# Performance work log

Measured on AMD Instinct MI355X. Metric: run time of the kernel, lower is better.

The kernel has to match this reference:

```python
import jax, jax.numpy as jnp
import numpy as np

B, T, D_IN, H, NUM_CLASSES = 1024, 512, 4, 64, 3
G = 4 * H  # gates: i, f, g, o (PyTorch order)


def setup_inputs() -> dict:
    key = jax.random.key(0)
    ks = jax.random.split(key, 32)
    s = 0.1  # small init scale, like PyTorch's 1/sqrt(H) uniform
    inp = {"x": jax.random.normal(ks[0], (B, T, D_IN), jnp.float32)}
    i = 1
    for l in range(4):
        d = D_IN if l == 0 else H
        inp[f"w_ih_{l}"] = s * jax.random.normal(ks[i], (G, d), jnp.float32); i += 1
        inp[f"w_hh_{l}"] = s * jax.random.normal(ks[i], (G, H), jnp.float32); i += 1
        inp[f"b_ih_{l}"] = s * jax.random.normal(ks[i], (G,), jnp.float32); i += 1
        inp[f"b_hh_{l}"] = s * jax.random.normal(ks[i], (G,), jnp.float32); i += 1
    inp["fc1_w"] = s * jax.random.normal(ks[i], (H // 2, H), jnp.float32); i += 1
    inp["fc1_b"] = s * jax.random.normal(ks[i], (H // 2,), jnp.float32); i += 1
    inp["fc2_w"] = s * jax.random.normal(ks[i], (NUM_CLASSES, H // 2), jnp.float32); i += 1
    inp["fc2_b"] = s * jax.random.normal(ks[i], (NUM_CLASSES,), jnp.float32)
    return inp


def _lstm_layer(x, w_ih, w_hh, b_ih, b_hh):
    # x: [B, T, d_in] -> [B, T, H]; PyTorch gate order i, f, g, o.
    b, t, _ = x.shape
    # Precompute input contribution for all timesteps in one GEMM.
    pre = jnp.einsum('btd,gd->tbg', x, w_ih) + (b_ih + b_hh)  # [T, B, 4H]
    h0 = jnp.zeros((b, H), x.dtype)
    c0 = jnp.zeros((b, H), x.dtype)

    def step(carry, p):
        h, c = carry
        gates = p + h @ w_hh.T  # [B, 4H]
        i_g, f_g, g_g, o_g = jnp.split(gates, 4, axis=-1)
        i_g = jax.nn.sigmoid(i_g)
        f_g = jax.nn.sigmoid(f_g)
        g_g = jnp.tanh(g_g)
        o_g = jax.nn.sigmoid(o_g)
        c = f_g * c + i_g * g_g
        h = o_g * jnp.tanh(c)
        return (h, c), h

    _, hs = jax.lax.scan(step, (h0, c0), pre)  # hs: [T, B, H]
    return hs.transpose(1, 0, 2)


def reference(x,
              w_ih_0, w_hh_0, b_ih_0, b_hh_0,
              w_ih_1, w_hh_1, b_ih_1, b_hh_1,
              w_ih_2, w_hh_2, b_ih_2, b_hh_2,
              w_ih_3, w_hh_3, b_ih_3, b_hh_3,
              fc1_w, fc1_b, fc2_w, fc2_b):
    layers = [(w_ih_0, w_hh_0, b_ih_0, b_hh_0),
              (w_ih_1, w_hh_1, b_ih_1, b_hh_1),
              (w_ih_2, w_hh_2, b_ih_2, b_hh_2),
              (w_ih_3, w_hh_3, b_ih_3, b_hh_3)]
    h = x
    for (wi, wh, bi, bh) in layers:
        h = _lstm_layer(h, wi, wh, bi, bh)
    last = h[:, -1, :]                         # [B, H]
    z = jax.nn.relu(last @ fc1_w.T + fc1_b)    # [B, H//2]
    logits = z @ fc2_w.T + fc2_b               # [B, 3]
    return jax.nn.softmax(logits, axis=1)
```

## Files before the change

### kernel.cpp

```cpp
#include <hip/hip_runtime.h>


#define TLEN 512
#define NCH  64
#define AG   __HIP_MEMORY_SCOPE_AGENT
#define SPIN_CAP 2000000
#define LOG2E 1.44269504f
#define TWOLOG2E 2.88539008f

typedef __bf16 bf16x8 __attribute__((ext_vector_type(8)));
typedef float  f32x4  __attribute__((ext_vector_type(4)));

struct Params {
  const float* x;
  const float* wih[4]; const float* whh[4];
  const float* bih[4]; const float* bhh[4];
  const float* fc1w; const float* fc1b;
  const float* fc2w; const float* fc2b;
  float* out; char* ws;
  int CAP; int CM;
};

__device__ __forceinline__ bf16x8 bfzero() {
  union { unsigned long long u[2]; bf16x8 v; } z; z.u[0] = 0ull; z.u[1] = 0ull; return z.v;
}
__device__ __forceinline__ float fast_sigmoid(float x) {
  return __builtin_amdgcn_rcpf(1.f + __expf(-x));
}
__device__ __forceinline__ float fast_tanh(float x) {
  float e = __expf(2.f * x);
  return 1.f - 2.f * __builtin_amdgcn_rcpf(e + 1.f);
}
__device__ __forceinline__ void load_frag_pair(const unsigned short* sb, int l15, int quad,
                                               bf16x8& f0, bf16x8& f1) {
  const unsigned long long* a = (const unsigned long long*)(sb + l15 * 64 + quad * 8);
  const unsigned long long* b = (const unsigned long long*)(sb + l15 * 64 + 32 + quad * 8);
  union { bf16x8 v; unsigned long long u[2]; } c0, c1;
  c0.u[0] = __hip_atomic_load(&a[0], __ATOMIC_RELAXED, AG);
  c0.u[1] = __hip_atomic_load(&a[1], __ATOMIC_RELAXED, AG);
  c1.u[0] = __hip_atomic_load(&b[0], __ATOMIC_RELAXED, AG);
  c1.u[1] = __hip_atomic_load(&b[1], __ATOMIC_RELAXED, AG);
  f0 = c0.v; f1 = c1.v;
}

__global__ __launch_bounds__(512, 1) void lstm_split(Params p)
{
  const int bid   = blockIdx.x;
  const int role  = bid >> 6;
  const int chunk = bid & 63;
  const int b0    = chunk * 16;
  const int tid   = threadIdx.x;
  const int wave  = tid >> 6;
  const int grp   = wave >> 2;
  const int w     = wave & 3;
  const int lane  = tid & 63;
  const int quad  = lane >> 4;
  const int l15   = lane & 15;
  const int L     = role * 2 + grp;

  __shared__ __bf16 tiles[2][2][1024];
  __shared__ float  s_fc1w[2048];
  __shared__ float  s_z[512];
  __shared__ float  s_fc1b[32];
  __shared__ float  s_fc2w[96];
  __shared__ float  s_fc2b[3];

  int* flagp = (int*)p.ws + chunk * 16;
  int* ackp  = (int*)(p.ws + 16 * 1024) + chunk * 16;
  unsigned short* ringc = (unsigned short*)(p.ws + 32 * 1024) + (size_t)chunk * p.CAP * 1024;
  const int CAP = p.CAP, CM = p.CM;

  bf16x8 wf[4][4];
  float  bias[4];
  {
    const float gsc[4] = { -LOG2E, -LOG2E, TWOLOG2E, -LOG2E };
    const float* wih = p.wih[L];
    const float* whh = p.whh[L];
    const float* bih = p.bih[L];
    const float* bhh = p.bhh[L];
#pragma unroll
    for (int g = 0; g < 4; g++) {
      const float sc = gsc[g];
      int n = g * 64 + w * 16 + l15;
      bias[g] = (bih[n] + bhh[n]) * sc;
      if (L == 0) {
        bf16x8 f = bfzero();
        if (quad == 0) {
#pragma unroll
          for (int j = 0; j < 4; j++) f[j] = (__bf16)(wih[n * 4 + j] * sc);
        }
        wf[g][0] = f; wf[g][1] = bfzero();
      } else {
#pragma unroll
        for (int q = 0; q < 2; q++) {
          const float* s = wih + n * 64 + q * 32 + quad * 8;
          bf16x8 f;
#pragma unroll
          for (int j = 0; j < 8; j++) f[j] = (__bf16)(s[j] * sc);
          wf[g][q] = f;
        }
      }
#pragma unroll
      for (int q = 0; q < 2; q++) {
        const float* s = whh + n * 64 + q * 32 + quad * 8;
        bf16x8 f;
#pragma unroll
        for (int j = 0; j < 8; j++) f[j] = (__bf16)(s[j] * sc);
        wf[g][2 + q] = f;
      }
    }
  }

  { int* ti = (int*)tiles; for (int i = tid; i < 2048; i += 512) ti[i] = 0; }
  float cst[4] = {0.f, 0.f, 0.f, 0.f};

  int W = -1000000000, f_pend = -1000000000;
  int ackW = -1000000000, a_pend = -1000000000;
  bf16x8 xA0 = bfzero(), xA1 = bfzero();
  bf16x8 xB0 = bfzero(), xB1 = bfzero();
  bf16x8 xC0 = bfzero(), xC1 = bfzero();
  float4 xraw = {0.f, 0.f, 0.f, 0.f};

  if (role == 0) {
    if (grp == 0 && quad == 0) {
      const float* xb = p.x + (size_t)(b0 + l15) * TLEN * 4;
      const float4 x0 = *(const float4*)(xb);
      const float4 x1 = *(const float4*)(xb + 4);
      xraw = *(const float4*)(xb + 8);
      bf16x8 f = bfzero();
      f[0] = (__bf16)x0.x; f[1] = (__bf16)x0.y; f[2] = (__bf16)x0.z; f[3] = (__bf16)x0.w;
      xA0 = f;
      bf16x8 g = bfzero();
      g[0] = (__bf16)x1.x; g[1] = (__bf16)x1.y; g[2] = (__bf16)x1.z; g[3] = (__bf16)x1.w;
      xB0 = g;
    }
  } else if (grp == 0) {
    int v = -1000000000, it = 0;
    do {
      if (lane == 0) v = __hip_atomic_load(flagp, __ATOMIC_ACQUIRE, AG);
      v = __shfl(v, 0);
      if (v >= 10) break;
      __builtin_amdgcn_s_sleep(1);
    } while (++it < SPIN_CAP);
    W = v;
    load_frag_pair(ringc,        l15, quad, xA0, xA1);
    load_frag_pair(ringc + 1024, l15, quad, xB0, xB1);
    load_frag_pair(ringc + 2048, l15, quad, xC0, xC1);
  }
  __syncthreads();

  const int SMAX = (role == 0) ? (TLEN + 2) : (TLEN + 1);
  for (int s = 0; s < SMAX; s++) {
    const int t  = s - grp;
    const int pr = s & 1, pw = pr ^ 1;
    unsigned hb[4];

    if ((unsigned)t < (unsigned)TLEN) {
      bf16x8 if0, if1;
      if (grp == 0) { if0 = xA0; if1 = xA1; }
      else {
        const __bf16* src = tiles[pr][0];
        int sg0 = quad ^ (l15 & 7);
        int sg1 = (4 + quad) ^ (l15 & 7);
        if0 = *(const bf16x8*)&src[l15 * 64 + sg0 * 8];
        if1 = *(const bf16x8*)&src[l15 * 64 + sg1 * 8];
      }
      bf16x8 hf0, hf1;
      {
        const __bf16* src = tiles[pr][grp];
        int sg0 = quad ^ (l15 & 7);
        int sg1 = (4 + quad) ^ (l15 & 7);
        hf0 = *(const bf16x8*)&src[l15 * 64 + sg0 * 8];
        hf1 = *(const bf16x8*)&src[l15 * 64 + sg1 * 8];
      }

      f32x4 acc[4];
#pragma unroll
      for (int g = 0; g < 4; g++) { f32x4 a = {bias[g], bias[g], bias[g], bias[g]}; acc[g] = a; }
      if (L == 0) {
#pragma unroll
        for (int g = 0; g < 4; g++)
          acc[g] = __builtin_amdgcn_mfma_f32_16x16x32_bf16(if0, wf[g][0], acc[g], 0, 0, 0);
      } else {
#pragma unroll
        for (int g = 0; g < 4; g++) {
          acc[g] = __builtin_amdgcn_mfma_f32_16x16x32_bf16(if0, wf[g][0], acc[g], 0, 0, 0);
          acc[g] = __builtin_amdgcn_mfma_f32_16x16x32_bf16(if1, wf[g][1], acc[g], 0, 0, 0);
        }
      }
#pragma unroll
      for (int g = 0; g < 4; g++) {
        acc[g] = __builtin_amdgcn_mfma_f32_16x16x32_bf16(hf0, wf[g][2], acc[g], 0, 0, 0);
        acc[g] = __builtin_amdgcn_mfma_f32_16x16x32_bf16(hf1, wf[g][3], acc[g], 0, 0, 0);
      }

      const int col = w * 16 + l15;
      __bf16* dst = tiles[pw][grp];
#pragma unroll
      for (int r = 0; r < 4; r++) {
        float ig = __builtin_amdgcn_rcpf(1.f + __builtin_amdgcn_exp2f(acc[0][r]));
        float fg = __builtin_amdgcn_rcpf(1.f + __builtin_amdgcn_exp2f(acc[1][r]));
        float gg = 1.f - 2.f * __builtin_amdgcn_rcpf(1.f + __builtin_amdgcn_exp2f(acc[2][r]));
        float og = __builtin_amdgcn_rcpf(1.f + __builtin_amdgcn_exp2f(acc[3][r]));
        float c  = fg * cst[r] + ig * gg;
        cst[r] = c;
        float th = 1.f - 2.f * __builtin_amdgcn_rcpf(1.f + __builtin_amdgcn_exp2f(TWOLOG2E * c));
        float h  = og * th;
        __bf16 hbf = (__bf16)h;
        union { __bf16 b; unsigned short s; } cv; cv.b = hbf;
        hb[r] = cv.s;
        int m  = quad * 4 + r;
        int sg = (col >> 3) ^ (m & 7);
        dst[m * 64 + sg * 8 + (col & 7)] = hbf;
      }
    }

    __syncthreads();

    if (role == 0) {
      if (grp == 0) {
        xA0 = xB0;
        if (quad == 0) {
          bf16x8 f = bfzero();
          f[0] = (__bf16)xraw.x; f[1] = (__bf16)xraw.y;
          f[2] = (__bf16)xraw.z; f[3] = (__bf16)xraw.w;
          xB0 = f;
          if (t + 3 < TLEN)
            xraw = *(const float4*)(p.x + ((size_t)(b0 + l15) * TLEN + (t + 3)) * 4);
        }
      }
      if (grp == 1 && (unsigned)t < (unsigned)TLEN) {
        int am = __shfl(a_pend, 0);
        if (am > ackW) ackW = am;
        if (lane == 0) a_pend = __hip_atomic_load(ackp, __ATOMIC_RELAXED, AG);
        if (t >= CAP && ackW < t - CAP + 1) {
          int v = ackW, it = 0;
          do {
            if (lane == 0) v = __hip_atomic_load(ackp, __ATOMIC_ACQUIRE, AG);
            v = __shfl(v, 0);
            if (v >= t - CAP + 1) break;
            __builtin_amdgcn_s_sleep(1);
          } while (++it < SPIN_CAP);
          ackW = v;
        }
        const int col = w * 16 + l15;
        unsigned* rdst = (unsigned*)(ringc + (size_t)(t & CM) * 1024);
#pragma unroll
        for (int r = 0; r < 4; r++) {
          unsigned v = hb[r];
          unsigned o = (unsigned)__shfl_xor((int)v, 1);
          if ((lane & 1) == 0) {
            int m = quad * 4 + r;
            __hip_atomic_store(&rdst[(m * 64 + col) >> 1], v | (o << 16), __ATOMIC_RELAXED, AG);
          }
        }
      }
      if (tid == 0 && s >= 2)
        __hip_atomic_store(flagp, s - 1, __ATOMIC_RELAXED, AG);
    } else {
      if (grp == 0) {
        int fm = __shfl(f_pend, 0);
        if (fm > W) W = fm;
        if (lane == 0) f_pend = __hip_atomic_load(flagp, __ATOMIC_RELAXED, AG);
        xA0 = xB0; xA1 = xB1; xB0 = xC0; xB1 = xC1;
        if (t + 3 < TLEN) {
          if (W < t + 4) {
            int v = W, it = 0;
            do {
              if (lane == 0) v = __hip_atomic_load(flagp, __ATOMIC_ACQUIRE, AG);
              v = __shfl(v, 0);
              if (v >= t + 4) break;
              __builtin_amdgcn_s_sleep(1);
            } while (++it < SPIN_CAP);
            W = v;
          }
          load_frag_pair(ringc + (size_t)((t + 3) & CM) * 1024, l15, quad, xC0, xC1);
        }
      }
      if (tid == 0)
        __hip_atomic_store(ackp, s + 2, __ATOMIC_RELAXED, AG);
    }
  }

  if (role == 1) {
    for (int i = tid; i < 2048; i += 512) s_fc1w[i] = p.fc1w[i];
    if (tid < 32) s_fc1b[tid] = p.fc1b[tid];
    if (tid < 96) s_fc2w[tid] = p.fc2w[tid];
    if (tid < 3)  s_fc2b[tid] = p.fc2b[tid];
    __syncthreads();
    {
      int m = tid >> 5, u = tid & 31;
      float sacc = s_fc1b[u];
      const float* wrow = &s_fc1w[u * 64];
      const __bf16* hfin = tiles[1][1];
#pragma unroll
      for (int k = 0; k < 64; k++) {
        int sg = (k >> 3) ^ (m & 7);
        sacc += (float)hfin[m * 64 + sg * 8 + (k & 7)] * wrow[k];
      }
      s_z[m * 32 + u] = fmaxf(sacc, 0.f);
    }
    __syncthreads();
    if (tid < 16) {
      int m = tid;
      float lg[3];
#pragma unroll
      for (int v = 0; v < 3; v++) {
        float sv = s_fc2b[v];
#pragma unroll
        for (int u = 0; u < 32; u++) sv += s_z[m * 32 + u] * s_fc2w[v * 32 + u];
        lg[v] = sv;
      }
      float mx = fmaxf(lg[0], fmaxf(lg[1], lg[2]));
      float e0 = __expf(lg[0] - mx), e1 = __expf(lg[1] - mx), e2 = __expf(lg[2] - mx);
      float inv = 1.f / (e0 + e1 + e2);
      float* o = p.out + (size_t)(b0 + m) * 3;
      o[0] = e0 * inv; o[1] = e1 * inv; o[2] = e2 * inv;
    }
  }
}

__global__ __launch_bounds__(1024) void lstm_fused(Params p)
{
  const int chunk = blockIdx.x;
  const int b0   = chunk * 16;
  const int tid  = threadIdx.x;
  const int wave = tid >> 6;
  const int L    = wave >> 2;
  const int w    = wave & 3;
  const int lane = tid & 63;
  const int quad = lane >> 4;
  const int l15  = lane & 15;

  __shared__ __bf16 tiles[2][5][16 * 64];
  __shared__ float  s_fc1w[2048];
  __shared__ float  s_z[512];
  __shared__ float  s_fc1b[32];
  __shared__ float  s_fc2w[96];
  __shared__ float  s_fc2b[3];

  bf16x8 wf[4][4];
  float  bias[4];
  {
    const float* wih = p.wih[L];
    const float* whh = p.whh[L];
    const float* bih = p.bih[L];
    const float* bhh = p.bhh[L];
#pragma unroll
    for (int g = 0; g < 4; g++) {
      int n = g * 64 + w * 16 + l15;
      bias[g] = bih[n] + bhh[n];
      if (L == 0) {
        bf16x8 f = bfzero();
        if (quad == 0) {
#pragma unroll
          for (int j = 0; j < 4; j++) f[j] = (__bf16)wih[n * 4 + j];
        }
        wf[g][0] = f; wf[g][1] = bfzero();
      } else {
#pragma unroll
        for (int q = 0; q < 2; q++) {
          const float* s = wih + n * 64 + q * 32 + quad * 8;
          bf16x8 f;
#pragma unroll
          for (int j = 0; j < 8; j++) f[j] = (__bf16)s[j];
          wf[g][q] = f;
        }
      }
#pragma unroll
      for (int q = 0; q < 2; q++) {
        const float* s = whh + n * 64 + q * 32 + quad * 8;
        bf16x8 f;
#pragma unroll
        for (int j = 0; j < 8; j++) f[j] = (__bf16)s[j];
        wf[g][2 + q] = f;
      }
    }
  }

  { int* ti = (int*)tiles; for (int i = tid; i < 5120; i += 1024) ti[i] = 0; }
  float cst[4] = {0.f, 0.f, 0.f, 0.f};

  if (wave == 0 && quad == 0) {
    const float4 xv = *(const float4*)(p.x + ((size_t)(b0 + l15) * TLEN) * 4);
    __bf16 v[4] = {(__bf16)xv.x, (__bf16)xv.y, (__bf16)xv.z, (__bf16)xv.w};
    *(float2*)&tiles[0][0][l15 * 64 + (l15 & 7) * 8] = *(float2*)v;
  }
  __syncthreads();

  for (int s = 0; s < TLEN + 3; s++) {
    const int t  = s - L;
    const int pr = s & 1;
    const int pw = pr ^ 1;

    if ((unsigned)t < (unsigned)TLEN) {
      const __bf16* in  = tiles[pr][L];
      const __bf16* own = tiles[pr][L + 1];
      const int sg0 = quad ^ (l15 & 7);
      const int sg1 = (4 + quad) ^ (l15 & 7);
      bf16x8 xf0 = *(const bf16x8*)&in [l15 * 64 + sg0 * 8];
      bf16x8 xf1 = *(const bf16x8*)&in [l15 * 64 + sg1 * 8];
      bf16x8 hf0 = *(const bf16x8*)&own[l15 * 64 + sg0 * 8];
      bf16x8 hf1 = *(const bf16x8*)&own[l15 * 64 + sg1 * 8];

      f32x4 acc[4];
#pragma unroll
      for (int g = 0; g < 4; g++) { f32x4 a = {bias[g], bias[g], bias[g], bias[g]}; acc[g] = a; }
#pragma unroll
      for (int g = 0; g < 4; g++) {
        acc[g] = __builtin_amdgcn_mfma_f32_16x16x32_bf16(xf0, wf[g][0], acc[g], 0, 0, 0);
        acc[g] = __builtin_amdgcn_mfma_f32_16x16x32_bf16(xf1, wf[g][1], acc[g], 0, 0, 0);
        acc[g] = __builtin_amdgcn_mfma_f32_16x16x32_bf16(hf0, wf[g][2], acc[g], 0, 0, 0);
        acc[g] = __builtin_amdgcn_mfma_f32_16x16x32_bf16(hf1, wf[g][3], acc[g], 0, 0, 0);
      }

      if (wave == 0 && quad == 0 && t + 1 < TLEN) {
        const float4 xv = *(const float4*)(p.x + ((size_t)(b0 + l15) * TLEN + (t + 1)) * 4);
        __bf16 v[4] = {(__bf16)xv.x, (__bf16)xv.y, (__bf16)xv.z, (__bf16)xv.w};
        *(float2*)&tiles[pw][0][l15 * 64 + (l15 & 7) * 8] = *(float2*)v;
      }

      const int col = w * 16 + l15;
      __bf16* dst = tiles[pw][L + 1];
#pragma unroll
      for (int r = 0; r < 4; r++) {
        float ig = fast_sigmoid(acc[0][r]);
        float fg = fast_sigmoid(acc[1][r]);
        float gg = fast_tanh(acc[2][r]);
        float og = fast_sigmoid(acc[3][r]);
        float c = fg * cst[r] + ig * gg;
        cst[r] = c;
        float h = og * fast_tanh(c);
        int m  = quad * 4 + r;
        int sg = (col >> 3) ^ (m & 7);
        dst[m * 64 + sg * 8 + (col & 7)] = (__bf16)h;
      }
    }
    __syncthreads();
  }

  for (int i = tid; i < 2048; i += 1024) s_fc1w[i] = p.fc1w[i];
  if (tid < 32) s_fc1b[tid] = p.fc1b[tid];
  if (tid < 96) s_fc2w[tid] = p.fc2w[tid];
  if (tid < 3)  s_fc2b[tid] = p.fc2b[tid];
  __syncthreads();
  if (tid < 512) {
    int m = tid >> 5, u = tid & 31;
    float sacc = s_fc1b[u];
    const float* wrow = &s_fc1w[u * 64];
    const __bf16* hfin = tiles[1][4];
#pragma unroll
    for (int k = 0; k < 64; k++) {
      int sg = (k >> 3) ^ (m & 7);
      sacc += (float)hfin[m * 64 + sg * 8 + (k & 7)] * wrow[k];
    }
    s_z[m * 32 + u] = fmaxf(sacc, 0.f);
  }
  __syncthreads();
  if (tid < 16) {
    int m = tid;
    float lg[3];
#pragma unroll
    for (int v = 0; v < 3; v++) {
      float sv = s_fc2b[v];
#pragma unroll
      for (int u = 0; u < 32; u++) sv += s_z[m * 32 + u] * s_fc2w[v * 32 + u];
      lg[v] = sv;
    }
    float mx = fmaxf(lg[0], fmaxf(lg[1], lg[2]));
    float e0 = __expf(lg[0] - mx), e1 = __expf(lg[1] - mx), e2 = __expf(lg[2] - mx);
    float inv = 1.f / (e0 + e1 + e2);
    float* o = p.out + (size_t)(b0 + m) * 3;
    o[0] = e0 * inv; o[1] = e1 * inv; o[2] = e2 * inv;
  }
}

extern "C" void kernel_launch(void* const* d_in, const int* in_sizes, int n_in,
                              void* d_out, int out_size, void* d_ws, size_t ws_size,
                              hipStream_t stream)
{
  (void)in_sizes; (void)n_in; (void)out_size;
  Params p;
  p.x = (const float*)d_in[0];
  for (int l = 0; l < 4; l++) {
    p.wih[l] = (const float*)d_in[1 + 4 * l];
    p.whh[l] = (const float*)d_in[2 + 4 * l];
    p.bih[l] = (const float*)d_in[3 + 4 * l];
    p.bhh[l] = (const float*)d_in[4 + 4 * l];
  }
  p.fc1w = (const float*)d_in[17];
  p.fc1b = (const float*)d_in[18];
  p.fc2w = (const float*)d_in[19];
  p.fc2b = (const float*)d_in[20];
  p.out = (float*)d_out;
  p.ws  = (char*)d_ws;

  const size_t avail = (ws_size > 32768) ? (ws_size - 32768) : 0;
  int CAP = 1;
  while (CAP < 64 && (size_t)(CAP * 2) * (NCH * 2048ull) <= avail) CAP <<= 1;

  if (CAP >= 16) {
    p.CAP = CAP; p.CM = CAP - 1;
    hipLaunchKernelGGL(lstm_split, dim3(128), dim3(512), 65536, stream, p);
  } else {
    p.CAP = 0; p.CM = 0;
    hipLaunchKernelGGL(lstm_fused, dim3(NCH), dim3(1024), 0, stream, p);
  }
}
```

Before: 881.0 us.

## Process two batch chunks per block in split LSTM kernel

The two-role pipelined LSTM kernel now handles two 16-row batch chunks per block, so the grid shrinks from 128 to 64 blocks. Each block interleaves two independent recurrences per timestep, which lets MFMA and transcendental latency of one chunk overlap with the other, and one flag/ack handshake now covers both chunks. The cost is a longer per-step critical path, more registers and shared memory per block, and fewer CUs in use. The forced 64 KB dynamic shared-memory allocation is dropped and the spin cap is lowered.

Result: slower. 1.314 ms (+49.2%).

```diff
diff --git a/kernel.cpp b/kernel.cpp
--- a/kernel.cpp
+++ b/kernel.cpp
@@ -4,7 +4,7 @@
 #define TLEN 512
 #define NCH  64
 #define AG   __HIP_MEMORY_SCOPE_AGENT
-#define SPIN_CAP 2000000
+#define SPIN_CAP 1500000
 #define LOG2E 1.44269504f
 #define TWOLOG2E 2.88539008f
 
@@ -43,12 +43,11 @@
   f0 = c0.v; f1 = c1.v;
 }
 
-__global__ __launch_bounds__(512, 1) void lstm_split(Params p)
+__global__ __launch_bounds__(512, 1) void lstm_split2(Params p)
 {
   const int bid   = blockIdx.x;
-  const int role  = bid >> 6;
-  const int chunk = bid & 63;
-  const int b0    = chunk * 16;
+  const int role  = bid >> 5;
+  const int k     = bid & 31;
   const int tid   = threadIdx.x;
   const int wave  = tid >> 6;
   const int grp   = wave >> 2;
@@ -57,17 +56,21 @@
   const int quad  = lane >> 4;
   const int l15   = lane & 15;
   const int L     = role * 2 + grp;
-
-  __shared__ __bf16 tiles[2][2][1024];
+  const int cc[2] = { k, k + 32 };
+
+  __shared__ __bf16 tiles[2][2][2][1024];
   __shared__ float  s_fc1w[2048];
-  __shared__ float  s_z[512];
+  __shared__ float  s_z[1024];
   __shared__ float  s_fc1b[32];
   __shared__ float  s_fc2w[96];
   __shared__ float  s_fc2b[3];
 
-  int* flagp = (int*)p.ws + chunk * 16;
-  int* ackp  = (int*)(p.ws + 16 * 1024) + chunk * 16;
-  unsigned short* ringc = (unsigned short*)(p.ws + 32 * 1024) + (size_t)chunk * p.CAP * 1024;
+  int* flagp = (int*)p.ws + cc[0] * 16;
+  int* ackp  = (int*)(p.ws + 16 * 1024) + cc[0] * 16;
+  unsigned short* ringb = (unsigned short*)(p.ws + 32 * 1024);
+  unsigned short* ring[2];
+  ring[0] = ringb + (size_t)cc[0] * p.CAP * 1024;
+  ring[1] = ringb + (size_t)cc[1] * p.CAP * 1024;
   const int CAP = p.CAP, CM = p.CM;
 
   bf16x8 wf[4][4];
@@ -111,28 +114,36 @@
     }
   }
 
-  { int* ti = (int*)tiles; for (int i = tid; i < 2048; i += 512) ti[i] = 0; }
-  float cst[4] = {0.f, 0.f, 0.f, 0.f};
+  { int* ti = (int*)tiles; for (int i = tid; i < 4096; i += 512) ti[i] = 0; }
+  float cst[2][4] = {{0.f,0.f,0.f,0.f},{0.f,0.f,0.f,0.f}};
 
   int W = -1000000000, f_pend = -1000000000;
   int ackW = -1000000000, a_pend = -1000000000;
-  bf16x8 xA0 = bfzero(), xA1 = bfzero();
-  bf16x8 xB0 = bfzero(), xB1 = bfzero();
-  bf16x8 xC0 = bfzero(), xC1 = bfzero();
-  float4 xraw = {0.f, 0.f, 0.f, 0.f};
+  bf16x8 xA0[2], xA1[2], xB0[2], xB1[2], xC0[2], xC1[2];
+#pragma unroll
+  for (int ch = 0; ch < 2; ch++) {
+    xA0[ch] = bfzero(); xA1[ch] = bfzero();
+    xB0[ch] = bfzero(); xB1[ch] = bfzero();
+    xC0[ch] = bfzero(); xC1[ch] = bfzero();
+  }
+  float4 xraw[2];
+  xraw[0] = {0.f,0.f,0.f,0.f}; xraw[1] = {0.f,0.f,0.f,0.f};
 
   if (role == 0) {
     if (grp == 0 && quad == 0) {
-      const float* xb = p.x + (size_t)(b0 + l15) * TLEN * 4;
-      const float4 x0 = *(const float4*)(xb);
-      const float4 x1 = *(const float4*)(xb + 4);
-      xraw = *(const float4*)(xb + 8);
-      bf16x8 f = bfzero();
-      f[0] = (__bf16)x0.x; f[1] = (__bf16)x0.y; f[2] = (__bf16)x0.z; f[3] = (__bf16)x0.w;
-      xA0 = f;
-      bf16x8 g = bfzero();
-      g[0] = (__bf16)x1.x; g[1] = (__bf16)x1.y; g[2] = (__bf16)x1.z; g[3] = (__bf16)x1.w;
-      xB0 = g;
+#pragma unroll
+      for (int ch = 0; ch < 2; ch++) {
+        const float* xb = p.x + (size_t)(cc[ch] * 16 + l15) * TLEN * 4;
+        const float4 x0 = *(const float4*)(xb);
+        const float4 x1 = *(const float4*)(xb + 4);
+        xraw[ch] = *(const float4*)(xb + 8);
+        bf16x8 f = bfzero();
+        f[0] = (__bf16)x0.x; f[1] = (__bf16)x0.y; f[2] = (__bf16)x0.z; f[3] = (__bf16)x0.w;
+        xA0[ch] = f;
+        bf16x8 g = bfzero();
+        g[0] = (__bf16)x1.x; g[1] = (__bf16)x1.y; g[2] = (__bf16)x1.z; g[3] = (__bf16)x1.w;
+        xB0[ch] = g;
+      }
     }
   } else if (grp == 0) {
     int v = -1000000000, it = 0;
@@ -143,9 +154,12 @@
       __builtin_amdgcn_s_sleep(1);
     } while (++it < SPIN_CAP);
     W = v;
-    load_frag_pair(ringc,        l15, quad, xA0, xA1);
-    load_frag_pair(ringc + 1024, l15, quad, xB0, xB1);
-    load_frag_pair(ringc + 2048, l15, quad, xC0, xC1);
+#pragma unroll
+    for (int ch = 0; ch < 2; ch++) {
+      load_frag_pair(ring[ch],        l15, quad, xA0[ch], xA1[ch]);
+      load_frag_pair(ring[ch] + 1024, l15, quad, xB0[ch], xB1[ch]);
+      load_frag_pair(ring[ch] + 2048, l15, quad, xC0[ch], xC1[ch]);
+    }
   }
   __syncthreads();
 
@@ -153,65 +167,68 @@
   for (int s = 0; s < SMAX; s++) {
     const int t  = s - grp;
     const int pr = s & 1, pw = pr ^ 1;
-    unsigned hb[4];
+    unsigned hb[2][4];
 
     if ((unsigned)t < (unsigned)TLEN) {
-      bf16x8 if0, if1;
-      if (grp == 0) { if0 = xA0; if1 = xA1; }
-      else {
-        const __bf16* src = tiles[pr][0];
-        int sg0 = quad ^ (l15 & 7);
-        int sg1 = (4 + quad) ^ (l15 & 7);
-        if0 = *(const bf16x8*)&src[l15 * 64 + sg0 * 8];
-        if1 = *(const bf16x8*)&src[l15 * 64 + sg1 * 8];
-      }
-      bf16x8 hf0, hf1;
-      {
-        const __bf16* src = tiles[pr][grp];
-        int sg0 = quad ^ (l15 & 7);
-        int sg1 = (4 + quad) ^ (l15 & 7);
-        hf0 = *(const bf16x8*)&src[l15 * 64 + sg0 * 8];
-        hf1 = *(const bf16x8*)&src[l15 * 64 + sg1 * 8];
-      }
-
-      f32x4 acc[4];
-#pragma unroll
-      for (int g = 0; g < 4; g++) { f32x4 a = {bias[g], bias[g], bias[g], bias[g]}; acc[g] = a; }
-      if (L == 0) {
-#pragma unroll
-        for (int g = 0; g < 4; g++)
-          acc[g] = __builtin_amdgcn_mfma_f32_16x16x32_bf16(if0, wf[g][0], acc[g], 0, 0, 0);
-      } else {
+#pragma unroll
+      for (int ch = 0; ch < 2; ch++) {
+        bf16x8 if0, if1;
+        if (grp == 0) { if0 = xA0[ch]; if1 = xA1[ch]; }
+        else {
+          const __bf16* src = tiles[pr][0][ch];
+          int sg0 = quad ^ (l15 & 7);
+          int sg1 = (4 + quad) ^ (l15 & 7);
+          if0 = *(const bf16x8*)&src[l15 * 64 + sg0 * 8];
+          if1 = *(const bf16x8*)&src[l15 * 64 + sg1 * 8];
+        }
+        bf16x8 hf0, hf1;
+        {
+          const __bf16* src = tiles[pr][grp][ch];
+          int sg0 = quad ^ (l15 & 7);
+          int sg1 = (4 + quad) ^ (l15 & 7);
+          hf0 = *(const bf16x8*)&src[l15 * 64 + sg0 * 8];
+          hf1 = *(const bf16x8*)&src[l15 * 64 + sg1 * 8];
+        }
+
+        f32x4 acc[4];
+#pragma unroll
+        for (int g = 0; g < 4; g++) { f32x4 a = {bias[g], bias[g], bias[g], bias[g]}; acc[g] = a; }
+        if (L == 0) {
+#pragma unroll
+          for (int g = 0; g < 4; g++)
+            acc[g] = __builtin_amdgcn_mfma_f32_16x16x32_bf16(if0, wf[g][0], acc[g], 0, 0, 0);
+        } else {
+#pragma unroll
+          for (int g = 0; g < 4; g++) {
+            acc[g] = __builtin_amdgcn_mfma_f32_16x16x32_bf16(if0, wf[g][0], acc[g], 0, 0, 0);
+            acc[g] = __builtin_amdgcn_mfma_f32_16x16x32_bf16(if1, wf[g][1], acc[g], 0, 0, 0);
+          }
+        }
 #pragma unroll
         for (int g = 0; g < 4; g++) {
-          acc[g] = __builtin_amdgcn_mfma_f32_16x16x32_bf16(if0, wf[g][0], acc[g], 0, 0, 0);
-          acc[g] = __builtin_amdgcn_mfma_f32_16x16x32_bf16(if1, wf[g][1], acc[g], 0, 0, 0);
-        }
-      }
-#pragma unroll
-      for (int g = 0; g < 4; g++) {
-        acc[g] = __builtin_amdgcn_mfma_f32_16x16x32_bf16(hf0, wf[g][2], acc[g], 0, 0, 0);
-        acc[g] = __builtin_amdgcn_mfma_f32_16x16x32_bf16(hf1, wf[g][3], acc[g], 0, 0, 0);
-      }
-
-      const int col = w * 16 + l15;
-      __bf16* dst = tiles[pw][grp];
-#pragma unroll
-      for (int r = 0; r < 4; r++) {
-        float ig = __builtin_amdgcn_rcpf(1.f + __builtin_amdgcn_exp2f(acc[0][r]));
-        float fg = __builtin_amdgcn_rcpf(1.f + __builtin_amdgcn_exp2f(acc[1][r]));
-        float gg = 1.f - 2.f * __builtin_amdgcn_rcpf(1.f + __builtin_amdgcn_exp2f(acc[2][r]));
-        float og = __builtin_amdgcn_rcpf(1.f + __builtin_amdgcn_exp2f(acc[3][r]));
-        float c  = fg * cst[r] + ig * gg;
-        cst[r] = c;
-        float th = 1.f - 2.f * __builtin_amdgcn_rcpf(1.f + __builtin_amdgcn_exp2f(TWOLOG2E * c));
-        float h  = og * th;
-        __bf16 hbf = (__bf16)h;
-        union { __bf16 b; unsigned short s; } cv; cv.b = hbf;
-        hb[r] = cv.s;
-        int m  = quad * 4 + r;
-        int sg = (col >> 3) ^ (m & 7);
-        dst[m * 64 + sg * 8 + (col & 7)] = hbf;
+          acc[g] = __builtin_amdgcn_mfma_f32_16x16x32_bf16(hf0, wf[g][2], acc[g], 0, 0, 0);
+          acc[g] = __builtin_amdgcn_mfma_f32_16x16x32_bf16(hf1, wf[g][3], acc[g], 0, 0, 0);
+        }
+
+        const int col = w * 16 + l15;
+        __bf16* dst = tiles[pw][grp][ch];
+#pragma unroll
+        for (int r = 0; r < 4; r++) {
+          float ig = __builtin_amdgcn_rcpf(1.f + __builtin_amdgcn_exp2f(acc[0][r]));
+          float fg = __builtin_amdgcn_rcpf(1.f + __builtin_amdgcn_exp2f(acc[1][r]));
+          float gg = 1.f - 2.f * __builtin_amdgcn_rcpf(1.f + __builtin_amdgcn_exp2f(acc[2][r]));
+          float og = __builtin_amdgcn_rcpf(1.f + __builtin_amdgcn_exp2f(acc[3][r]));
+          float c  = fg * cst[ch][r] + ig * gg;
+          cst[ch][r] = c;
+          float th = 1.f - 2.f * __builtin_amdgcn_rcpf(1.f + __builtin_amdgcn_exp2f(TWOLOG2E * c));
+          float h  = og * th;
+          __bf16 hbf = (__bf16)h;
+          union { __bf16 b; unsigned short s; } cv; cv.b = hbf;
+          hb[ch][r] = cv.s;
+          int m  = quad * 4 + r;
+          int sg = (col >> 3) ^ (m & 7);
+          dst[m * 64 + sg * 8 + (col & 7)] = hbf;
+        }
       }
     }
 
@@ -219,14 +236,18 @@
 
     if (role == 0) {
       if (grp == 0) {
-        xA0 = xB0;
+#pragma unroll
+        for (int ch = 0; ch < 2; ch++) xA0[ch] = xB0[ch];
         if (quad == 0) {
-          bf16x8 f = bfzero();
-          f[0] = (__bf16)xraw.x; f[1] = (__bf16)xraw.y;
-          f[2] = (__bf16)xraw.z; f[3] = (__bf16)xraw.w;
-          xB0 = f;
-          if (t + 3 < TLEN)
-            xraw = *(const float4*)(p.x + ((size_t)(b0 + l15) * TLEN + (t + 3)) * 4);
+#pragma unroll
+          for (int ch = 0; ch < 2; ch++) {
+            bf16x8 f = bfzero();
+            f[0] = (__bf16)xraw[ch].x; f[1] = (__bf16)xraw[ch].y;
+            f[2] = (__bf16)xraw[ch].z; f[3] = (__bf16)xraw[ch].w;
+            xB0[ch] = f;
+            if (t + 3 < TLEN)
+              xraw[ch] = *(const float4*)(p.x + ((size_t)(cc[ch] * 16 + l15) * TLEN + (t + 3)) * 4);
+          }
         }
       }
       if (grp == 1 && (unsigned)t < (unsigned)TLEN) {
@@ -244,14 +265,17 @@
           ackW = v;
         }
         const int col = w * 16 + l15;
-        unsigned* rdst = (unsigned*)(ringc + (size_t)(t & CM) * 1024);
-#pragma unroll
-        for (int r = 0; r < 4; r++) {
-          unsigned v = hb[r];
-          unsigned o = (unsigned)__shfl_xor((int)v, 1);
-          if ((lane & 1) == 0) {
-            int m = quad * 4 + r;
-            __hip_atomic_store(&rdst[(m * 64 + col) >> 1], v | (o << 16), __ATOMIC_RELAXED, AG);
+#pragma unroll
+        for (int ch = 0; ch < 2; ch++) {
+          unsigned* rdst = (unsigned*)(ring[ch] + (size_t)(t & CM) * 1024);
+#pragma unroll
+          for (int r = 0; r < 4; r++) {
+            unsigned v = hb[ch][r];
+            unsigned o = (unsigned)__shfl_xor((int)v, 1);
+            if ((lane & 1) == 0) {
+              int m = quad * 4 + r;
+              __hip_atomic_store(&rdst[(m * 64 + col) >> 1], v | (o << 16), __ATOMIC_RELAXED, AG);
+            }
           }
         }
       }
@@ -262,7 +286,11 @@
         int fm = __shfl(f_pend, 0);
         if (fm > W) W = fm;
         if (lane == 0) f_pend = __hip_atomic_load(flagp, __ATOMIC_RELAXED, AG);
-        xA0 = xB0; xA1 = xB1; xB0 = xC0; xB1 = xC1;
+#pragma unroll
+        for (int ch = 0; ch < 2; ch++) {
+          xA0[ch] = xB0[ch]; xA1[ch] = xB1[ch];
+          xB0[ch] = xC0[ch]; xB1[ch] = xC1[ch];
+        }
         if (t + 3 < TLEN) {
           if (W < t + 4) {
             int v = W, it = 0;
@@ -274,7 +302,9 @@
             } while (++it < SPIN_CAP);
             W = v;
           }
-          load_frag_pair(ringc + (size_t)((t + 3) & CM) * 1024, l15, quad, xC0, xC1);
+#pragma unroll
+          for (int ch = 0; ch < 2; ch++)
+            load_frag_pair(ring[ch] + (size_t)((t + 3) & CM) * 1024, l15, quad, xC0[ch], xC1[ch]);
         }
       }
       if (tid == 0)
@@ -288,21 +318,22 @@
     if (tid < 96) s_fc2w[tid] = p.fc2w[tid];
     if (tid < 3)  s_fc2b[tid] = p.fc2b[tid];
     __syncthreads();
-    {
-      int m = tid >> 5, u = tid & 31;
+    for (int i = tid; i < 1024; i += 512) {
+      int m = i >> 5, u = i & 31;
+      int ch = m >> 4, mm = m & 15;
       float sacc = s_fc1b[u];
       const float* wrow = &s_fc1w[u * 64];
-      const __bf16* hfin = tiles[1][1];
-#pragma unroll
-      for (int k = 0; k < 64; k++) {
-        int sg = (k >> 3) ^ (m & 7);
-        sacc += (float)hfin[m * 64 + sg * 8 + (k & 7)] * wrow[k];
+      const __bf16* hfin = tiles[1][1][ch];
+#pragma unroll
+      for (int kk = 0; kk < 64; kk++) {
+        int sg = (kk >> 3) ^ (mm & 7);
+        sacc += (float)hfin[mm * 64 + sg * 8 + (kk & 7)] * wrow[kk];
       }
       s_z[m * 32 + u] = fmaxf(sacc, 0.f);
     }
     __syncthreads();
-    if (tid < 16) {
-      int m = tid;
+    if (tid < 32) {
+      int m = tid, ch = m >> 4, mm = m & 15;
       float lg[3];
 #pragma unroll
       for (int v = 0; v < 3; v++) {
@@ -314,7 +345,7 @@
       float mx = fmaxf(lg[0], fmaxf(lg[1], lg[2]));
       float e0 = __expf(lg[0] - mx), e1 = __expf(lg[1] - mx), e2 = __expf(lg[2] - mx);
       float inv = 1.f / (e0 + e1 + e2);
-      float* o = p.out + (size_t)(b0 + m) * 3;
+      float* o = p.out + (size_t)(cc[ch] * 16 + mm) * 3;
       o[0] = e0 * inv; o[1] = e1 * inv; o[2] = e2 * inv;
     }
   }
@@ -450,9 +481,9 @@
     const float* wrow = &s_fc1w[u * 64];
     const __bf16* hfin = tiles[1][4];
 #pragma unroll
-    for (int k = 0; k < 64; k++) {
-      int sg = (k >> 3) ^ (m & 7);
-      sacc += (float)hfin[m * 64 + sg * 8 + (k & 7)] * wrow[k];
+    for (int kk = 0; kk < 64; kk++) {
+      int sg = (kk >> 3) ^ (m & 7);
+      sacc += (float)hfin[m * 64 + sg * 8 + (kk & 7)] * wrow[kk];
     }
     s_z[m * 32 + u] = fmaxf(sacc, 0.f);
   }
@@ -501,7 +532,7 @@
 
   if (CAP >= 16) {
     p.CAP = CAP; p.CM = CAP - 1;
-    hipLaunchKernelGGL(lstm_split, dim3(128), dim3(512), 65536, stream, p);
+    hipLaunchKernelGGL(lstm_split2, dim3(64), dim3(512), 0, stream, p);
   } else {
     p.CAP = 0; p.CM = 0;
     hipLaunchKernelGGL(lstm_fused, dim3(NCH), dim3(1024), 0, stream, p);
```
